# Performance work log

Hardware: AMD Instinct MI355X
Metric: run time of the kernel (lower is better)

Reference implementation:

```python
import jax, jax.numpy as jnp
import numpy as np
from jax import lax

# ---- fixed configuration (matches init_kwargs / input_specs) ----
L, E, V, F, HU, HL, S = 32, 1024, 2048, 8, 128, 2, 7
D0, D1R, D1E = 512, 129, 640
D = S + 1                      # path dimension = num_slices + 1
SIGLEN = D + D * D + D * D * D # iisignature.siglength(8, 3) = 584
FINAL = F * 2 * SIGLEN         # 9344
EPS = 1e-5                     # BatchNorm eps


def _bn(x, g, b):
    # BatchNorm1d in training mode: biased batch statistics over axis 0
    mu = x.mean(0)
    var = x.var(0)
    return (x - mu) / jnp.sqrt(var + EPS) * g + b


def _mlp(x, Win, bin_, gin, betain, Wh, bh, gh, betah, Wout, bout, gout, betaout):
    # eigf: Linear+BN+ReLU blocks, 1 -> HU -> ... -> HU -> 1
    h = jax.nn.relu(_bn(x @ Win.T + bin_, gin, betain))
    for l in range(HL):
        h = jax.nn.relu(_bn(h @ Wh[l].T + bh[l], gh[l], betah[l]))
    o = jax.nn.relu(_bn(h @ Wout.T + bout, gout, betaout))
    return o[:, 0]


# ---- path signature, level 3, via Chen's identity (replaces iisignature.sig) ----
def _seg(dx):
    s1 = dx
    s2 = jnp.outer(s1, dx).reshape(-1) * 0.5
    s3 = jnp.outer(s2, dx).reshape(-1) / 3.0
    return (s1, s2, s3)


def _chen(Sg, T):
    s1, s2, s3 = Sg
    t1, t2, t3 = T
    r1 = s1 + t1
    r2 = s2 + t2 + jnp.outer(s1, t1).reshape(-1)
    r3 = s3 + t3 + jnp.outer(s1, t2).reshape(-1) + jnp.outer(s2, t1).reshape(-1)
    return (r1, r2, r3)


def _sig3(path):  # path [P, D] -> [SIGLEN]
    dX = path[1:] - path[:-1]

    def step(Sg, dx):
        return _chen(Sg, _seg(dx)), None

    Sg, _ = lax.scan(step, _seg(dX[0]), dX[1:])
    return jnp.concatenate(Sg)


def _diagram_sig(vals, W_proj, b_proj):
    # Conv1d(1, S, kernel=2, stride=2) == pairwise projection; then sort, prepend time axis
    pairs = vals.reshape(-1, 2)                      # [P, 2]
    P = pairs.shape[0]
    proj = jnp.einsum('pk,sk->sp', pairs, W_proj[:, 0, :]) + b_proj[:, None]  # [S, P]
    proj = jnp.sort(proj, axis=-1)
    t = jnp.arange(P, dtype=vals.dtype) / (P * (P + 1) / 2.0)
    path = jnp.concatenate([t[None, :], proj], axis=0).T  # [P, D]
    return _sig3(path)


def setup_inputs() -> dict:
    key = jax.random.key(0)
    ks = iter(jax.random.split(key, 16))
    nrm = lambda kk, shp, sc: jax.random.normal(kk, shp, jnp.float32) * sc
    inp = {
        "eigenvalues": jax.random.uniform(next(ks), (L, E), jnp.float32),
        "eigenvectors_sq": jax.random.uniform(next(ks), (L, E, V), jnp.float32) / E,
        "dgm0": jax.random.randint(next(ks), (L, F, D0), 0, V, jnp.int32),
        "dgm1rel": jax.random.randint(next(ks), (L, F, D1R), 0, V, jnp.int32),
        "dgm1ext": jax.random.randint(next(ks), (L, F, D1E), 0, V, jnp.int32),
        "mlp_Win": nrm(next(ks), (F, HU, 1), 1.0),
        "mlp_bin": jnp.zeros((F, HU), jnp.float32),
        "mlp_gin": jnp.ones((F, HU), jnp.float32),
        "mlp_betain": jnp.zeros((F, HU), jnp.float32),
        "mlp_Wh": nrm(next(ks), (F, HL, HU, HU), 1.0 / np.sqrt(HU)),
        "mlp_bh": jnp.zeros((F, HL, HU), jnp.float32),
        "mlp_gh": jnp.ones((F, HL, HU), jnp.float32),
        "mlp_betah": jnp.zeros((F, HL, HU), jnp.float32),
        "mlp_Wout": nrm(next(ks), (F, 1, HU), 1.0 / np.sqrt(HU)),
        "mlp_bout": jnp.zeros((F, 1), jnp.float32),
        "mlp_gout": jnp.ones((F, 1), jnp.float32),
        "mlp_betaout": jnp.zeros((F, 1), jnp.float32),
        "W_proj": nrm(next(ks), (S, 1, 2), 0.7),
        "b_proj": jnp.zeros((S,), jnp.float32),
        "W_fin": nrm(next(ks), (1, FINAL), 1.0 / np.sqrt(FINAL)),
        "b_fin": jnp.zeros((1,), jnp.float32),
        "g_fin": jnp.ones((1,), jnp.float32),
        "beta_fin": jnp.zeros((1,), jnp.float32),
    }
    return inp


def reference(eigenvalues, eigenvectors_sq, dgm0, dgm1rel, dgm1ext,
              mlp_Win, mlp_bin, mlp_gin, mlp_betain,
              mlp_Wh, mlp_bh, mlp_gh, mlp_betah,
              mlp_Wout, mlp_bout, mlp_gout, mlp_betaout,
              W_proj, b_proj, W_fin, b_fin, g_fin, beta_fin):
    flat = eigenvalues.reshape(-1, 1)  # [L*E, 1], sample-major like the torch flatten
    evs = jax.vmap(lambda *p: _mlp(flat, *p))(
        mlp_Win, mlp_bin, mlp_gin, mlp_betain,
        mlp_Wh, mlp_bh, mlp_gh, mlp_betah,
        mlp_Wout, mlp_bout, mlp_gout, mlp_betaout)  # [F, L*E]
    # per-sample filtration values: evs_transformed[:, slice_i] @ eigvecsq_i
    f = jnp.einsum('fle,lev->lfv', evs.reshape(F, L, E), eigenvectors_sq)  # [L, F, V]
    fv = f.reshape(L * F, V)
    d0 = jnp.take_along_axis(fv, dgm0.reshape(L * F, D0), axis=1)
    rel = jnp.take_along_axis(fv, dgm1rel.reshape(L * F, D1R), axis=1)
    # torch.arange(len-1, 0, -1): reversed, dropping element 0
    Dgm0 = jnp.concatenate([d0, rel[:, 1:][:, ::-1]], axis=1)  # [L*F, 640]
    Dgm1 = jnp.take_along_axis(fv, dgm1ext.reshape(L * F, D1E), axis=1)
    sig0 = jax.vmap(lambda v: _diagram_sig(v, W_proj, b_proj))(Dgm0)  # [L*F, SIGLEN]
    sig1 = jax.vmap(lambda v: _diagram_sig(v, W_proj, b_proj))(Dgm1)
    x = jnp.concatenate([sig0, sig1], axis=-1).reshape(L, FINAL)
    out = x @ W_fin.T + b_fin  # dropout p=0.0 -> identity
    return _bn(out, g_fin, beta_fin)  # [L, 1]
```

## Files before the change

### kernel.cpp

```cpp
#include <hip/hip_runtime.h>
#include <cfloat>
#include <math.h>

#define N_SAMP 32768
#define FF 8
#define HU 128
#define EE 1024
#define VV 2048
#define PP 320
#define SIGLEN 584
#define FINAL_W 9344

typedef unsigned short u16;
typedef unsigned int u32;
typedef short s16x8 __attribute__((ext_vector_type(8)));
typedef float f32x4 __attribute__((ext_vector_type(4)));

__device__ __forceinline__ u16 f2bf(float v) {
  u32 u = __float_as_uint(v);
  return (u16)((u + 0x7fffu + ((u >> 16) & 1u)) >> 16);
}
__device__ __forceinline__ float bf2f(u16 h) {
  return __uint_as_float(((u32)h) << 16);
}
__device__ __forceinline__ void split3(float v, u16& h, u16& m, u16& l) {
  h = f2bf(v);
  float r = v - bf2f(h);
  m = f2bf(r);
  float r2 = r - bf2f(m);
  l = f2bf(r2);
}

__device__ __forceinline__ double wave_red(double v) {
#pragma unroll
  for (int off = 32; off > 0; off >>= 1) v += __shfl_xor(v, off, 64);
  return v;
}

__global__ __launch_bounds__(256) void k_prep(const float* __restrict__ W,
                                              u16* __restrict__ Hh, u16* __restrict__ Hm,
                                              u16* __restrict__ Hl,
                                              const float* __restrict__ x,
                                              double* __restrict__ xp,
                                              double* __restrict__ stats_zero) {
  __shared__ double r1[4], r2[4];
  const int bid = blockIdx.x, tid = threadIdx.x;
  if (bid < 1024) {
    int i = bid * 256 + tid;
    u16 h, m, l;
    split3(W[i], h, m, l);
    Hh[i] = h; Hm[i] = m; Hl[i] = l;
  } else if (bid < 1056) {
    int b = bid - 1024;
    double s1 = 0.0, s2 = 0.0;
    int base = b * 1024 + tid;
#pragma unroll
    for (int r = 0; r < 4; ++r) {
      double v = (double)x[base + r * 256];
      s1 += v; s2 += v * v;
    }
    s1 = wave_red(s1); s2 = wave_red(s2);
    int wave = tid >> 6, lane = tid & 63;
    if (lane == 0) { r1[wave] = s1; r2[wave] = s2; }
    __syncthreads();
    if (tid == 0) {
      xp[b * 2 + 0] = r1[0] + r1[1] + r1[2] + r1[3];
      xp[b * 2 + 1] = r2[0] + r2[1] + r2[2] + r2[3];
    }
  } else {
    int q = (bid - 1056) * 256 + tid;
    stats_zero[q] = 0.0;
    if (bid == 1056 && tid < 16) stats_zero[4096 + tid] = 0.0;
  }
}

template<int MODE>
__global__ __launch_bounds__(256, 2)
void k_mgemm(const float* __restrict__ Ain,
             const double* __restrict__ xp,
             const float* __restrict__ w_in,
             const float* __restrict__ g_in,
             const float* __restrict__ beta_in,
             const double* __restrict__ stats_in,
             const float* __restrict__ gM1,
             const float* __restrict__ betaM1,
             const u16* __restrict__ Wh_,
             const u16* __restrict__ Wm_,
             const u16* __restrict__ Wl_,
             const float* __restrict__ bb, int bstride,
             float* __restrict__ Yt_out,
             double* __restrict__ stats) {
  __shared__ u16 SB[6][128 * 40];
  __shared__ float p0[HU], p1[HU], biasl[HU], xl[HU];
  u16* Ah = SB[0]; u16* Am = SB[1]; u16* Al = SB[2];
  u16* Bh = SB[3]; u16* Bm = SB[4]; u16* Bl = SB[5];

  const int tid = threadIdx.x;
  const int f = blockIdx.y;
  const int m0 = blockIdx.x * 128;
  const int lane = tid & 63, ln = tid & 15, quad = (tid >> 4) & 3, wave = tid >> 6;

  if (tid < HU) {
    biasl[tid] = bb[(size_t)f * bstride + tid];
    if (MODE == 0) {
      double S1 = 0.0, S2 = 0.0;
#pragma unroll
      for (int r = 0; r < 32; ++r) { S1 += xp[r * 2]; S2 += xp[r * 2 + 1]; }
      double mx = S1 * (1.0 / 32768.0);
      double vx = S2 * (1.0 / 32768.0) - mx * mx;
      if (vx < 0) vx = 0;
      float w = w_in[f * HU + tid];
      double inv = 1.0 / sqrt((double)w * (double)w * vx + 1e-5);
      float sj = (float)inv * g_in[f * HU + tid] * w;
      p0[tid] = sj;
      p1[tid] = beta_in[f * HU + tid] - (float)mx * sj;
      xl[tid] = Ain[m0 + tid];
    } else {
      int idx = f * HU + tid;
      double S1 = stats_in[idx * 2 + 0], S2 = stats_in[idx * 2 + 1];
      double mean = S1 * (1.0 / 32768.0);
      double var = S2 * (1.0 / 32768.0) - mean * mean;
      if (var < 0) var = 0;
      double inv = 1.0 / sqrt(var + 1e-5);
      float gg = gM1[f * 256 + tid];
      float scv = (float)inv * gg;
      p0[tid] = scv;
      p1[tid] = betaM1[f * 256 + tid] - (float)mean * scv;
    }
  }

  f32x4 acc[2][8];
#pragma unroll
  for (int mt = 0; mt < 2; ++mt)
#pragma unroll
    for (int u = 0; u < 8; ++u) acc[mt][u] = (f32x4){0.f, 0.f, 0.f, 0.f};

  __syncthreads();

  for (int kk = 0; kk < 128; kk += 32) {
    if (MODE == 0) {
      const int m = tid >> 1, kh = (tid & 1) * 16;
      const float xv = xl[m];
      u32 ph[8], pm[8], pl[8];
#pragma unroll
      for (int jp = 0; jp < 8; ++jp) {
        u16 h0, m_0, l0, h1, m_1, l1;
        int k = kh + jp * 2;
        split3(fmaxf(fmaf(xv, p0[kk + k], p1[kk + k]), 0.f), h0, m_0, l0);
        split3(fmaxf(fmaf(xv, p0[kk + k + 1], p1[kk + k + 1]), 0.f), h1, m_1, l1);
        ph[jp] = (u32)h0 | ((u32)h1 << 16);
        pm[jp] = (u32)m_0 | ((u32)m_1 << 16);
        pl[jp] = (u32)l0 | ((u32)l1 << 16);
      }
      int off = m * 40 + kh;
      *(uint4*)&Ah[off] = make_uint4(ph[0], ph[1], ph[2], ph[3]);
      *(uint4*)&Ah[off + 8] = make_uint4(ph[4], ph[5], ph[6], ph[7]);
      *(uint4*)&Am[off] = make_uint4(pm[0], pm[1], pm[2], pm[3]);
      *(uint4*)&Am[off + 8] = make_uint4(pm[4], pm[5], pm[6], pm[7]);
      *(uint4*)&Al[off] = make_uint4(pl[0], pl[1], pl[2], pl[3]);
      *(uint4*)&Al[off + 8] = make_uint4(pl[4], pl[5], pl[6], pl[7]);
    } else {
#pragma unroll
      for (int r = 0; r < 4; ++r) {
        int flat = tid + r * 256;
        int m = flat & 127, kq = flat >> 7;
        const float* src = Ain + ((size_t)(f * HU + kk + kq * 4)) * N_SAMP + m0 + m;
        u32 ph[2], pm[2], pl[2];
#pragma unroll
        for (int ip = 0; ip < 2; ++ip) {
          int k = kq * 4 + ip * 2;
          float v0 = fmaxf(fmaf(src[(size_t)(ip * 2) * N_SAMP], p0[kk + k], p1[kk + k]), 0.f);
          float v1 = fmaxf(fmaf(src[(size_t)(ip * 2 + 1) * N_SAMP], p0[kk + k + 1], p1[kk + k + 1]), 0.f);
          u16 h0, m_0, l0, h1, m_1, l1;
          split3(v0, h0, m_0, l0);
          split3(v1, h1, m_1, l1);
          ph[ip] = (u32)h0 | ((u32)h1 << 16);
          pm[ip] = (u32)m_0 | ((u32)m_1 << 16);
          pl[ip] = (u32)l0 | ((u32)l1 << 16);
        }
        int off = m * 40 + kq * 4;
        *(uint2*)&Ah[off] = make_uint2(ph[0], ph[1]);
        *(uint2*)&Am[off] = make_uint2(pm[0], pm[1]);
        *(uint2*)&Al[off] = make_uint2(pl[0], pl[1]);
      }
    }
#pragma unroll
    for (int r = 0; r < 2; ++r) {
      int flat = tid + r * 256;
      int n = flat >> 2, c = flat & 3;
      size_t g = (size_t)f * (2 * HU * HU) + (size_t)n * HU + kk + c * 8;
      int off = n * 40 + c * 8;
      *(uint4*)&Bh[off] = *(const uint4*)&Wh_[g];
      *(uint4*)&Bm[off] = *(const uint4*)&Wm_[g];
      *(uint4*)&Bl[off] = *(const uint4*)&Wl_[g];
    }
    __syncthreads();
    s16x8 af0[3], af1[3];
    {
      int r0 = (wave * 32 + ln) * 40 + quad * 8;
      int r1 = (wave * 32 + 16 + ln) * 40 + quad * 8;
      af0[0] = *(const s16x8*)&Ah[r0]; af0[1] = *(const s16x8*)&Am[r0]; af0[2] = *(const s16x8*)&Al[r0];
      af1[0] = *(const s16x8*)&Ah[r1]; af1[1] = *(const s16x8*)&Am[r1]; af1[2] = *(const s16x8*)&Al[r1];
    }
#pragma unroll
    for (int u = 0; u < 8; ++u) {
      int bo = (u * 16 + ln) * 40 + quad * 8;
      s16x8 bh = *(const s16x8*)&Bh[bo];
      s16x8 bm = *(const s16x8*)&Bm[bo];
      s16x8 bl = *(const s16x8*)&Bl[bo];
      f32x4 a0 = acc[0][u], a1 = acc[1][u];
      a0 = __builtin_amdgcn_mfma_f32_16x16x32_bf16(af0[0], bh, a0, 0, 0, 0);
      a1 = __builtin_amdgcn_mfma_f32_16x16x32_bf16(af1[0], bh, a1, 0, 0, 0);
      a0 = __builtin_amdgcn_mfma_f32_16x16x32_bf16(af0[1], bh, a0, 0, 0, 0);
      a1 = __builtin_amdgcn_mfma_f32_16x16x32_bf16(af1[1], bh, a1, 0, 0, 0);
      a0 = __builtin_amdgcn_mfma_f32_16x16x32_bf16(af0[0], bm, a0, 0, 0, 0);
      a1 = __builtin_amdgcn_mfma_f32_16x16x32_bf16(af1[0], bm, a1, 0, 0, 0);
      a0 = __builtin_amdgcn_mfma_f32_16x16x32_bf16(af0[2], bh, a0, 0, 0, 0);
      a1 = __builtin_amdgcn_mfma_f32_16x16x32_bf16(af1[2], bh, a1, 0, 0, 0);
      a0 = __builtin_amdgcn_mfma_f32_16x16x32_bf16(af0[1], bm, a0, 0, 0, 0);
      a1 = __builtin_amdgcn_mfma_f32_16x16x32_bf16(af1[1], bm, a1, 0, 0, 0);
      a0 = __builtin_amdgcn_mfma_f32_16x16x32_bf16(af0[0], bl, a0, 0, 0, 0);
      a1 = __builtin_amdgcn_mfma_f32_16x16x32_bf16(af1[0], bl, a1, 0, 0, 0);
      acc[0][u] = a0; acc[1][u] = a1;
    }
    __syncthreads();
  }

  float cs1[8], cs2[8];
#pragma unroll
  for (int u = 0; u < 8; ++u) { cs1[u] = 0.f; cs2[u] = 0.f; }
#pragma unroll
  for (int u = 0; u < 8; ++u) {
    float b = biasl[u * 16 + ln];
#pragma unroll
    for (int mt = 0; mt < 2; ++mt) {
#pragma unroll
      for (int reg = 0; reg < 4; ++reg) {
        float v = acc[mt][u][reg] + b;
        acc[mt][u][reg] = v;
        cs1[u] += v;
        cs2[u] = fmaf(v, v, cs2[u]);
      }
      float4 st = make_float4(acc[mt][u][0], acc[mt][u][1], acc[mt][u][2], acc[mt][u][3]);
      *(float4*)&Yt_out[((size_t)(f * HU + u * 16 + ln)) * N_SAMP + m0 + wave * 32 + mt * 16 + quad * 4] = st;
    }
  }
  float* red1 = (float*)&SB[0][0];
  float* red2 = red1 + 2048;
  int wq = wave * 4 + quad;
#pragma unroll
  for (int u = 0; u < 8; ++u) {
    red1[wq * 128 + u * 16 + ln] = cs1[u];
    red2[wq * 128 + u * 16 + ln] = cs2[u];
  }
  __syncthreads();
  {
    int which = tid >> 7, n = tid & 127;
    const float* rp = which ? red2 : red1;
    float s = 0.f;
#pragma unroll
    for (int r = 0; r < 16; ++r) s += rp[r * 128 + n];
    atomicAdd(&stats[(f * HU + n) * 2 + which], (double)s);
  }
}

__global__ __launch_bounds__(256, 4) void k_outlayer(const float* __restrict__ Yt,
                                                     const double* __restrict__ stats2,
                                                     const float* __restrict__ gh,
                                                     const float* __restrict__ betah,
                                                     const float* __restrict__ Wout,
                                                     const float* __restrict__ bout,
                                                     float* __restrict__ evs_pre,
                                                     double* __restrict__ stats3) {
  __shared__ float wj[HU], scl[HU], shl[HU];
  const int tid = threadIdx.x;
  const int f = blockIdx.y;
  const int i = blockIdx.x * 256 + tid;
  if (tid < HU) {
    wj[tid] = Wout[f * HU + tid];
    int idx = f * HU + tid;
    double S1 = stats2[idx * 2 + 0], S2 = stats2[idx * 2 + 1];
    double mean = S1 * (1.0 / 32768.0);
    double var = S2 * (1.0 / 32768.0) - mean * mean;
    if (var < 0) var = 0;
    double inv = 1.0 / sqrt(var + 1e-5);
    float gg = gh[128 + f * 256 + tid];
    float scv = (float)inv * gg;
    scl[tid] = scv;
    shl[tid] = betah[128 + f * 256 + tid] - (float)mean * scv;
  }
  __syncthreads();
  const float* base = Yt + (size_t)f * HU * N_SAMP + i;
  float acc = 0.f;
#pragma unroll
  for (int j = 0; j < HU; ++j) {
    float y = base[(size_t)j * N_SAMP];
    acc = fmaf(fmaxf(fmaf(y, scl[j], shl[j]), 0.f), wj[j], acc);
  }
  float yo = acc + bout[f];
  evs_pre[(size_t)f * N_SAMP + i] = yo;
  double v = (double)yo;
  double s1 = wave_red(v), s2 = wave_red(v * v);
  __shared__ double r1[4], r2[4];
  int wave = tid >> 6, lane = tid & 63;
  if (lane == 0) { r1[wave] = s1; r2[wave] = s2; }
  __syncthreads();
  if (tid == 0) atomicAdd(&stats3[f * 2 + 0], r1[0] + r1[1] + r1[2] + r1[3]);
  if (tid == 1) atomicAdd(&stats3[f * 2 + 1], r2[0] + r2[1] + r2[2] + r2[3]);
}

__global__ __launch_bounds__(256) void k_einsum(const float* __restrict__ evs_pre,
                                                const double* __restrict__ stats3,
                                                const float* __restrict__ gout,
                                                const float* __restrict__ betaout,
                                                const float* __restrict__ eig,
                                                float* __restrict__ fv) {
  __shared__ float ev[FF * EE];
  __shared__ float scl3[FF], shl3[FF];
  const int tid = threadIdx.x;
  const int l = blockIdx.y;
  const int v0 = blockIdx.x * 256;
  if (tid < FF) {
    double S1 = stats3[tid * 2 + 0], S2 = stats3[tid * 2 + 1];
    double mean = S1 * (1.0 / 32768.0);
    double var = S2 * (1.0 / 32768.0) - mean * mean;
    if (var < 0) var = 0;
    double inv = 1.0 / sqrt(var + 1e-5);
    float gg = gout[tid];
    float scv = (float)inv * gg;
    scl3[tid] = scv;
    shl3[tid] = betaout[tid] - (float)mean * scv;
  }
  __syncthreads();
#pragma unroll
  for (int r = 0; r < 32; ++r) {
    int q = tid + r * 256;
    int f = q >> 10, e = q & 1023;
    float y = evs_pre[(size_t)f * N_SAMP + l * EE + e];
    ev[q] = fmaxf(fmaf(y, scl3[f], shl3[f]), 0.f);
  }
  __syncthreads();
  const float* up = eig + (size_t)l * EE * VV + v0 + tid;
  float acc[8] = {0, 0, 0, 0, 0, 0, 0, 0};
  for (int e0 = 0; e0 < EE; e0 += 32) {
    float u[32];
#pragma unroll
    for (int t = 0; t < 32; ++t) u[t] = up[(size_t)(e0 + t) * VV];
#pragma unroll
    for (int t = 0; t < 32; ++t) {
#pragma unroll
      for (int f = 0; f < 8; ++f) acc[f] = fmaf(ev[f * EE + e0 + t], u[t], acc[f]);
    }
  }
#pragma unroll
  for (int f = 0; f < 8; ++f) fv[((size_t)(l * FF + f)) * VV + v0 + tid] = acc[f];
}

__global__ __launch_bounds__(256) void k_diagram(const float* __restrict__ fv,
                                                 const int* __restrict__ dgm0,
                                                 const int* __restrict__ dgm1rel,
                                                 const int* __restrict__ dgm1ext,
                                                 const float* __restrict__ Wp,
                                                 const float* __restrict__ bp,
                                                 float* __restrict__ xbuf) {
  __shared__ float vals[640];
  __shared__ float ps[7 * 512];
  __shared__ float dXl[320][8];
  const int tid = threadIdx.x;
  const int bid = blockIdx.x;
  const int row = bid >> 1;
  const int c = bid & 1;
  const float* fvr = fv + (size_t)row * VV;

  for (int k = tid; k < 640; k += 256) {
    int idx;
    if (c == 0) idx = (k < 512) ? dgm0[(size_t)row * 512 + k] : dgm1rel[(size_t)row * 129 + (640 - k)];
    else        idx = dgm1ext[(size_t)row * 640 + k];
    vals[k] = fvr[idx];
  }
  __syncthreads();
  for (int q = tid; q < 7 * 512; q += 256) {
    int s = q >> 9, p = q & 511;
    float pv = 3.402823466e+38f;
    if (p < PP) pv = fmaf(Wp[2 * s + 1], vals[2 * p + 1], fmaf(Wp[2 * s], vals[2 * p], bp[s]));
    ps[s * 512 + p] = pv;
  }
  for (int k = 2; k <= 512; k <<= 1) {
    for (int j = k >> 1; j > 0; j >>= 1) {
      __syncthreads();
      for (int q = tid; q < 1792; q += 256) {
        int s = q >> 8, ip = q & 255;
        int i = ((ip & ~(j - 1)) << 1) | (ip & (j - 1));
        int p2 = i | j;
        float a = ps[s * 512 + i], b = ps[s * 512 + p2];
        bool up = ((i & k) == 0);
        if ((a > b) == up) { ps[s * 512 + i] = b; ps[s * 512 + p2] = a; }
      }
    }
  }
  __syncthreads();
  for (int q = tid; q < 319 * 8; q += 256) {
    int p = q >> 3, d = q & 7;
    dXl[p][d] = (d == 0) ? (1.0f / 51360.0f)
                         : ps[(d - 1) * 512 + p + 1] - ps[(d - 1) * 512 + p];
  }
  __syncthreads();
  {
    const int a = tid >> 5, b = (tid >> 2) & 7, dp = tid & 3;
    float s1a = 0.f, s2r = 0.f, s3r0 = 0.f, s3r1 = 0.f;
    for (int p = 0; p < 319; ++p) {
      float dxa = dXl[p][a];
      float dxb = dXl[p][b];
      float2 dd = *(const float2*)&dXl[p][dp * 2];
      float coefA = fmaf(dxa, (1.f / 3.f), s1a);
      float w = fmaf(0.5f * dxb, coefA, s2r);
      s2r = fmaf(dxb, fmaf(0.5f, dxa, s1a), s2r);
      s3r0 = fmaf(w, dd.x, s3r0);
      s3r1 = fmaf(w, dd.y, s3r1);
      s1a += dxa;
    }
    const int l = row >> 3, ff = row & 7;
    float* xr = xbuf + (size_t)l * FINAL_W + ff * (2 * SIGLEN) + c * SIGLEN;
    if (b == 0 && dp == 0) xr[a] = s1a;
    if (dp == 0) xr[8 + a * 8 + b] = s2r;
    float* s3p = xr + 72 + (a * 8 + b) * 8 + dp * 2;
    s3p[0] = s3r0;
    s3p[1] = s3r1;
  }
}

__global__ __launch_bounds__(256) void k_rowdot(const float* __restrict__ xbuf,
                                                const float* __restrict__ Wf,
                                                const float* __restrict__ bf,
                                                double* __restrict__ outpre) {
  const int tid = threadIdx.x, l = blockIdx.x;
  const float* xr = xbuf + (size_t)l * FINAL_W;
  double acc = 0.0;
  for (int k = tid; k < FINAL_W; k += 256) acc += (double)xr[k] * (double)Wf[k];
  acc = wave_red(acc);
  __shared__ double r[4];
  int wave = tid >> 6, lane = tid & 63;
  if (lane == 0) r[wave] = acc;
  __syncthreads();
  if (tid == 0) outpre[l] = r[0] + r[1] + r[2] + r[3] + (double)bf[0];
}

__global__ __launch_bounds__(64) void k_bnfin(const double* __restrict__ outpre,
                                              const float* __restrict__ g,
                                              const float* __restrict__ beta,
                                              float* __restrict__ dout) {
  int i = threadIdx.x;
  double v = (i < 32) ? outpre[i] : 0.0;
  double s1 = wave_red(v);
  double s2 = wave_red(v * v);
  double mean = s1 * (1.0 / 32.0);
  double var = s2 * (1.0 / 32.0) - mean * mean;
  if (var < 0) var = 0;
  double inv = 1.0 / sqrt(var + 1e-5);
  if (i < 32) dout[i] = (float)((v - mean) * inv * (double)g[0] + (double)beta[0]);
}

extern "C" void kernel_launch(void* const* d_in, const int* in_sizes, int n_in,
                              void* d_out, int out_size, void* d_ws, size_t ws_size,
                              hipStream_t stream) {
  const float* eig     = (const float*)d_in[0];
  const float* eigsq   = (const float*)d_in[1];
  const int*   dgm0    = (const int*)d_in[2];
  const int*   dgm1rel = (const int*)d_in[3];
  const int*   dgm1ext = (const int*)d_in[4];
  const float* Win     = (const float*)d_in[5];
  const float* gin     = (const float*)d_in[7];
  const float* betain  = (const float*)d_in[8];
  const float* Wh      = (const float*)d_in[9];
  const float* bh      = (const float*)d_in[10];
  const float* gh      = (const float*)d_in[11];
  const float* betah   = (const float*)d_in[12];
  const float* Wout    = (const float*)d_in[13];
  const float* bout    = (const float*)d_in[14];
  const float* gout    = (const float*)d_in[15];
  const float* betaout = (const float*)d_in[16];
  const float* Wp      = (const float*)d_in[17];
  const float* bp      = (const float*)d_in[18];
  const float* Wfin    = (const float*)d_in[19];
  const float* bfin    = (const float*)d_in[20];
  const float* gfin    = (const float*)d_in[21];
  const float* betafin = (const float*)d_in[22];

  char* ws = (char*)d_ws;
  float*  Yt      = (float*)(ws);
  float*  evs_pre = (float*)(ws + 134217728u);
  float*  fv      = (float*)(ws + 135266304u);
  float*  xbuf    = (float*)(ws + 137363456u);
  double* stats1  = (double*)(ws + 138576384u);
  double* stats2  = stats1 + 2048;
  double* stats3  = stats1 + 4096;
  double* xp      = stats1 + 4112;
  double* outpre  = stats1 + 4176;
  u16*    Whh     = (u16*)(ws + 138612736u);
  u16*    Whm     = (u16*)(ws + 139137024u);
  u16*    Whl     = (u16*)(ws + 139661312u);

  k_prep<<<1072, 256, 0, stream>>>(Wh, Whh, Whm, Whl, eig, xp, stats1);
  k_mgemm<0><<<dim3(256, FF), 256, 0, stream>>>(eig, xp, Win, gin, betain,
                                                nullptr, nullptr, nullptr,
                                                Whh, Whm, Whl,
                                                bh, 256, Yt, stats1);
  k_mgemm<1><<<dim3(256, FF), 256, 0, stream>>>(Yt, nullptr, nullptr, nullptr, nullptr,
                                                stats1, gh, betah,
                                                Whh + HU * HU, Whm + HU * HU, Whl + HU * HU,
                                                bh + 128, 256, Yt, stats2);
  k_outlayer<<<dim3(128, FF), 256, 0, stream>>>(Yt, stats2, gh, betah, Wout, bout,
                                                evs_pre, stats3);
  k_einsum<<<dim3(8, 32), 256, 0, stream>>>(evs_pre, stats3, gout, betaout, eigsq, fv);
  k_diagram<<<512, 256, 0, stream>>>(fv, dgm0, dgm1rel, dgm1ext, Wp, bp, xbuf);
  k_rowdot<<<32, 256, 0, stream>>>(xbuf, Wfin, bfin, outpre);
  k_bnfin<<<1, 64, 0, stream>>>(outpre, gfin, betafin, (float*)d_out);
}
```

Measured before the change: 688.7 us.

## Pre-pad weight tiles for direct LDS loads, vectorize outlayer/einsum, fuse final dot+BN

k_prep now writes the split bf16 weights in a pre-padded tile layout so k_mgemm can copy B tiles straight into LDS with global_load_lds instead of staging them through registers. k_outlayer processes two samples per thread with float2 loads, and k_einsum loads evs_pre with float4. The final row-dot and batch-norm kernels are folded into k_diagram using atomic accumulation and a last-block counter, which removes two launches and the xbuf round trip. This adds atomic-order nondeterminism and depends on the counter being zeroed in k_prep on every call.

```diff
diff --git a/kernel.cpp b/kernel.cpp
--- a/kernel.cpp
+++ b/kernel.cpp
@@ -37,19 +37,26 @@
   return v;
 }
 
+#define WPAD_ROW 40
+#define WPAD_CHUNK (128 * WPAD_ROW)
+#define WPAD_LAYER (4 * WPAD_CHUNK)
+#define WPAD_F (2 * WPAD_LAYER)
+#define WPAD_TOTAL (FF * WPAD_F)
+
 __global__ __launch_bounds__(256) void k_prep(const float* __restrict__ W,
                                               u16* __restrict__ Hh, u16* __restrict__ Hm,
                                               u16* __restrict__ Hl,
                                               const float* __restrict__ x,
-                                              double* __restrict__ xp,
-                                              double* __restrict__ stats_zero) {
+                                              double* __restrict__ D) {
   __shared__ double r1[4], r2[4];
   const int bid = blockIdx.x, tid = threadIdx.x;
   if (bid < 1024) {
     int i = bid * 256 + tid;
     u16 h, m, l;
     split3(W[i], h, m, l);
-    Hh[i] = h; Hm[i] = m; Hl[i] = l;
+    int k = i & 127, n = (i >> 7) & 127, f2l = i >> 14;
+    int out = f2l * WPAD_LAYER + (k >> 5) * WPAD_CHUNK + n * WPAD_ROW + (k & 31);
+    Hh[out] = h; Hm[out] = m; Hl[out] = l;
   } else if (bid < 1056) {
     int b = bid - 1024;
     double s1 = 0.0, s2 = 0.0;
@@ -64,13 +71,12 @@
     if (lane == 0) { r1[wave] = s1; r2[wave] = s2; }
     __syncthreads();
     if (tid == 0) {
-      xp[b * 2 + 0] = r1[0] + r1[1] + r1[2] + r1[3];
-      xp[b * 2 + 1] = r2[0] + r2[1] + r2[2] + r2[3];
+      D[b * 2 + 0] = r1[0] + r1[1] + r1[2] + r1[3];
+      D[b * 2 + 1] = r2[0] + r2[1] + r2[2] + r2[3];
     }
   } else {
     int q = (bid - 1056) * 256 + tid;
-    stats_zero[q] = 0.0;
-    if (bid == 1056 && tid < 16) stats_zero[4096 + tid] = 0.0;
+    if (q < 4145) D[64 + q] = 0.0;
   }
 }
 
@@ -138,6 +144,25 @@
   __syncthreads();
 
   for (int kk = 0; kk < 128; kk += 32) {
+    {
+      const int chunk = kk >> 5;
+      const u16* gH = Wh_ + (size_t)f * WPAD_F + chunk * WPAD_CHUNK;
+      const u16* gM = Wm_ + (size_t)f * WPAD_F + chunk * WPAD_CHUNK;
+      const u16* gL = Wl_ + (size_t)f * WPAD_F + chunk * WPAD_CHUNK;
+#pragma unroll
+      for (int t = 0; t < 8; ++t) {
+        int flat = wave + t * 4;
+        if (flat < 30) {
+          int L = (flat >= 20) ? 2 : (flat >= 10 ? 1 : 0);
+          int p = flat - L * 10;
+          const u16* g = (L == 0 ? gH : (L == 1 ? gM : gL)) + p * 512 + lane * 8;
+          u16* d = (L == 0 ? Bh : (L == 1 ? Bm : Bl)) + p * 512;
+          __builtin_amdgcn_global_load_lds(
+              (const __attribute__((address_space(1))) void*)g,
+              (__attribute__((address_space(3))) void*)d, 16, 0, 0);
+        }
+      }
+    }
     if (MODE == 0) {
       const int m = tid >> 1, kh = (tid & 1) * 16;
       const float xv = xl[m];
@@ -183,16 +208,6 @@
         *(uint2*)&Am[off] = make_uint2(pm[0], pm[1]);
         *(uint2*)&Al[off] = make_uint2(pl[0], pl[1]);
       }
-    }
-#pragma unroll
-    for (int r = 0; r < 2; ++r) {
-      int flat = tid + r * 256;
-      int n = flat >> 2, c = flat & 3;
-      size_t g = (size_t)f * (2 * HU * HU) + (size_t)n * HU + kk + c * 8;
-      int off = n * 40 + c * 8;
-      *(uint4*)&Bh[off] = *(const uint4*)&Wh_[g];
-      *(uint4*)&Bm[off] = *(const uint4*)&Wm_[g];
-      *(uint4*)&Bl[off] = *(const uint4*)&Wl_[g];
     }
     __syncthreads();
     s16x8 af0[3], af1[3];
@@ -275,7 +290,7 @@
   __shared__ float wj[HU], scl[HU], shl[HU];
   const int tid = threadIdx.x;
   const int f = blockIdx.y;
-  const int i = blockIdx.x * 256 + tid;
+  const int i = (blockIdx.x * 256 + tid) * 2;
   if (tid < HU) {
     wj[tid] = Wout[f * HU + tid];
     int idx = f * HU + tid;
@@ -290,17 +305,19 @@
     shl[tid] = betah[128 + f * 256 + tid] - (float)mean * scv;
   }
   __syncthreads();
-  const float* base = Yt + (size_t)f * HU * N_SAMP + i;
-  float acc = 0.f;
+  const float2* base2 = (const float2*)(Yt + (size_t)f * HU * N_SAMP + i);
+  float a0 = 0.f, a1 = 0.f;
 #pragma unroll
   for (int j = 0; j < HU; ++j) {
-    float y = base[(size_t)j * N_SAMP];
-    acc = fmaf(fmaxf(fmaf(y, scl[j], shl[j]), 0.f), wj[j], acc);
-  }
-  float yo = acc + bout[f];
-  evs_pre[(size_t)f * N_SAMP + i] = yo;
-  double v = (double)yo;
-  double s1 = wave_red(v), s2 = wave_red(v * v);
+    float2 y = base2[(size_t)j * (N_SAMP / 2)];
+    a0 = fmaf(fmaxf(fmaf(y.x, scl[j], shl[j]), 0.f), wj[j], a0);
+    a1 = fmaf(fmaxf(fmaf(y.y, scl[j], shl[j]), 0.f), wj[j], a1);
+  }
+  float yo0 = a0 + bout[f];
+  float yo1 = a1 + bout[f];
+  *(float2*)&evs_pre[(size_t)f * N_SAMP + i] = make_float2(yo0, yo1);
+  double v0 = (double)yo0, v1 = (double)yo1;
+  double s1 = wave_red(v0 + v1), s2 = wave_red(v0 * v0 + v1 * v1);
   __shared__ double r1[4], r2[4];
   int wave = tid >> 6, lane = tid & 63;
   if (lane == 0) { r1[wave] = s1; r2[wave] = s2; }
@@ -315,7 +332,7 @@
                                                 const float* __restrict__ betaout,
                                                 const float* __restrict__ eig,
                                                 float* __restrict__ fv) {
-  __shared__ float ev[FF * EE];
+  __shared__ __align__(16) float ev[FF * EE];
   __shared__ float scl3[FF], shl3[FF];
   const int tid = threadIdx.x;
   const int l = blockIdx.y;
@@ -333,11 +350,16 @@
   }
   __syncthreads();
 #pragma unroll
-  for (int r = 0; r < 32; ++r) {
-    int q = tid + r * 256;
-    int f = q >> 10, e = q & 1023;
-    float y = evs_pre[(size_t)f * N_SAMP + l * EE + e];
-    ev[q] = fmaxf(fmaf(y, scl3[f], shl3[f]), 0.f);
+  for (int r = 0; r < 8; ++r) {
+    int flat = tid + r * 256;
+    int fch = flat >> 8, e4 = (flat & 255) * 4;
+    float4 y = *(const float4*)&evs_pre[(size_t)fch * N_SAMP + l * EE + e4];
+    float sv = scl3[fch], hv = shl3[fch];
+    float* evp = &ev[fch * EE + e4];
+    evp[0] = fmaxf(fmaf(y.x, sv, hv), 0.f);
+    evp[1] = fmaxf(fmaf(y.y, sv, hv), 0.f);
+    evp[2] = fmaxf(fmaf(y.z, sv, hv), 0.f);
+    evp[3] = fmaxf(fmaf(y.w, sv, hv), 0.f);
   }
   __syncthreads();
   const float* up = eig + (size_t)l * EE * VV + v0 + tid;
@@ -362,10 +384,18 @@
                                                  const int* __restrict__ dgm1ext,
                                                  const float* __restrict__ Wp,
                                                  const float* __restrict__ bp,
-                                                 float* __restrict__ xbuf) {
+                                                 const float* __restrict__ Wf,
+                                                 const float* __restrict__ bf,
+                                                 const float* __restrict__ gfin,
+                                                 const float* __restrict__ betafin,
+                                                 double* __restrict__ outpre,
+                                                 unsigned int* __restrict__ cnt,
+                                                 float* __restrict__ dout) {
   __shared__ float vals[640];
   __shared__ float ps[7 * 512];
   __shared__ float dXl[320][8];
+  __shared__ double rr[4];
+  __shared__ unsigned int lastFlag;
   const int tid = threadIdx.x;
   const int bid = blockIdx.x;
   const int row = bid >> 1;
@@ -420,44 +450,35 @@
       s1a += dxa;
     }
     const int l = row >> 3, ff = row & 7;
-    float* xr = xbuf + (size_t)l * FINAL_W + ff * (2 * SIGLEN) + c * SIGLEN;
-    if (b == 0 && dp == 0) xr[a] = s1a;
-    if (dp == 0) xr[8 + a * 8 + b] = s2r;
-    float* s3p = xr + 72 + (a * 8 + b) * 8 + dp * 2;
-    s3p[0] = s3r0;
-    s3p[1] = s3r1;
-  }
-}
-
-__global__ __launch_bounds__(256) void k_rowdot(const float* __restrict__ xbuf,
-                                                const float* __restrict__ Wf,
-                                                const float* __restrict__ bf,
-                                                double* __restrict__ outpre) {
-  const int tid = threadIdx.x, l = blockIdx.x;
-  const float* xr = xbuf + (size_t)l * FINAL_W;
-  double acc = 0.0;
-  for (int k = tid; k < FINAL_W; k += 256) acc += (double)xr[k] * (double)Wf[k];
-  acc = wave_red(acc);
-  __shared__ double r[4];
-  int wave = tid >> 6, lane = tid & 63;
-  if (lane == 0) r[wave] = acc;
-  __syncthreads();
-  if (tid == 0) outpre[l] = r[0] + r[1] + r[2] + r[3] + (double)bf[0];
-}
-
-__global__ __launch_bounds__(64) void k_bnfin(const double* __restrict__ outpre,
-                                              const float* __restrict__ g,
-                                              const float* __restrict__ beta,
-                                              float* __restrict__ dout) {
-  int i = threadIdx.x;
-  double v = (i < 32) ? outpre[i] : 0.0;
-  double s1 = wave_red(v);
-  double s2 = wave_red(v * v);
-  double mean = s1 * (1.0 / 32.0);
-  double var = s2 * (1.0 / 32.0) - mean * mean;
-  if (var < 0) var = 0;
-  double inv = 1.0 / sqrt(var + 1e-5);
-  if (i < 32) dout[i] = (float)((v - mean) * inv * (double)g[0] + (double)beta[0]);
+    const int base = ff * (2 * SIGLEN) + c * SIGLEN;
+    double part = (double)s3r0 * (double)Wf[base + 72 + (a * 8 + b) * 8 + dp * 2]
+                + (double)s3r1 * (double)Wf[base + 72 + (a * 8 + b) * 8 + dp * 2 + 1];
+    if (dp == 0) part += (double)s2r * (double)Wf[base + 8 + a * 8 + b];
+    if (b == 0 && dp == 0) part += (double)s1a * (double)Wf[base + a];
+    part = wave_red(part);
+    int wv = tid >> 6, lnn = tid & 63;
+    if (lnn == 0) rr[wv] = part;
+    __syncthreads();
+    if (tid == 0) {
+      atomicAdd(&outpre[l], rr[0] + rr[1] + rr[2] + rr[3]);
+      __threadfence();
+      unsigned int old = atomicAdd(cnt, 1u);
+      lastFlag = (old == 511u) ? 1u : 0u;
+    }
+    __syncthreads();
+    if (lastFlag && tid < 64) {
+      __threadfence();
+      double v = 0.0;
+      if (tid < 32) v = ((volatile double*)outpre)[tid] + (double)bf[0];
+      double s1 = wave_red(v);
+      double s2 = wave_red(v * v);
+      double mean = s1 * (1.0 / 32.0);
+      double var = s2 * (1.0 / 32.0) - mean * mean;
+      if (var < 0) var = 0;
+      double inv = 1.0 / sqrt(var + 1e-5);
+      if (tid < 32) dout[tid] = (float)((v - mean) * inv * (double)gfin[0] + (double)betafin[0]);
+    }
+  }
 }
 
 extern "C" void kernel_launch(void* const* d_in, const int* in_sizes, int n_in,
@@ -490,29 +511,30 @@
   float*  Yt      = (float*)(ws);
   float*  evs_pre = (float*)(ws + 134217728u);
   float*  fv      = (float*)(ws + 135266304u);
-  float*  xbuf    = (float*)(ws + 137363456u);
-  double* stats1  = (double*)(ws + 138576384u);
-  double* stats2  = stats1 + 2048;
-  double* stats3  = stats1 + 4096;
-  double* xp      = stats1 + 4112;
-  double* outpre  = stats1 + 4176;
+  double* D       = (double*)(ws + 138576384u);
+  double* xp      = D;
+  double* stats1  = D + 64;
+  double* stats2  = D + 2112;
+  double* stats3  = D + 4160;
+  double* outpre  = D + 4176;
+  unsigned int* cnt = (unsigned int*)(D + 4208);
   u16*    Whh     = (u16*)(ws + 138612736u);
-  u16*    Whm     = (u16*)(ws + 139137024u);
-  u16*    Whl     = (u16*)(ws + 139661312u);
-
-  k_prep<<<1072, 256, 0, stream>>>(Wh, Whh, Whm, Whl, eig, xp, stats1);
+  u16*    Whm     = Whh + WPAD_TOTAL;
+  u16*    Whl     = Whm + WPAD_TOTAL;
+
+  k_prep<<<1073, 256, 0, stream>>>(Wh, Whh, Whm, Whl, eig, D);
   k_mgemm<0><<<dim3(256, FF), 256, 0, stream>>>(eig, xp, Win, gin, betain,
                                                 nullptr, nullptr, nullptr,
                                                 Whh, Whm, Whl,
                                                 bh, 256, Yt, stats1);
   k_mgemm<1><<<dim3(256, FF), 256, 0, stream>>>(Yt, nullptr, nullptr, nullptr, nullptr,
                                                 stats1, gh, betah,
-                                                Whh + HU * HU, Whm + HU * HU, Whl + HU * HU,
+                                                Whh + WPAD_LAYER, Whm + WPAD_LAYER, Whl + WPAD_LAYER,
                                                 bh + 128, 256, Yt, stats2);
-  k_outlayer<<<dim3(128, FF), 256, 0, stream>>>(Yt, stats2, gh, betah, Wout, bout,
-                                                evs_pre, stats3);
+  k_outlayer<<<dim3(64, FF), 256, 0, stream>>>(Yt, stats2, gh, betah, Wout, bout,
+                                               evs_pre, stats3);
   k_einsum<<<dim3(8, 32), 256, 0, stream>>>(evs_pre, stats3, gout, betaout, eigsq, fv);
-  k_diagram<<<512, 256, 0, stream>>>(fv, dgm0, dgm1rel, dgm1ext, Wp, bp, xbuf);
-  k_rowdot<<<32, 256, 0, stream>>>(xbuf, Wfin, bfin, outpre);
-  k_bnfin<<<1, 64, 0, stream>>>(outpre, gfin, betafin, (float*)d_out);
-}
+  k_diagram<<<512, 256, 0, stream>>>(fv, dgm0, dgm1rel, dgm1ext, Wp, bp,
+                                     Wfin, bfin, gfin, betafin, outpre, cnt,
+                                     (float*)d_out);
+}
```

After: 663.9 us. -3.6%, faster.
